# Kernel tuning notes

Hardware: AMD Instinct MI355X
Metric: run time of the kernel (lower is better)

## Reference

```python
import jax, jax.numpy as jnp
import numpy as np

EPS = 0.0  # GIN epsilon (train_eps=False)

def setup_inputs() -> dict:
    key = jax.random.key(0)
    k_x, k_e, k_w1, k_w2 = jax.random.split(key, 4)
    N, E, D = 100000, 625000, 128
    x = jax.random.normal(k_x, (N, D), dtype=jnp.float32)
    edge_index = jax.random.randint(k_e, (2, E), 0, N, dtype=jnp.int32)
    s = 1.0 / np.sqrt(D)
    W1 = jax.random.normal(k_w1, (D, D), dtype=jnp.float32) * s
    b1 = jnp.zeros((D,), dtype=jnp.float32)
    W2 = jax.random.normal(k_w2, (D, D), dtype=jnp.float32) * s
    b2 = jnp.zeros((D,), dtype=jnp.float32)
    return {"x": x, "edge_index": edge_index, "W1": W1, "b1": b1, "W2": W2, "b2": b2}

def reference(x, edge_index, W1, b1, W2, b2):
    # GINConv: out_i = MLP((1+eps)*x_i + sum_{j in N(i)} x_j)
    src = edge_index[0]
    dst = edge_index[1]
    agg = jax.ops.segment_sum(x[src], dst, num_segments=x.shape[0])  # [N, D]
    h = (1.0 + EPS) * x + agg
    # MLP: Linear -> ReLU -> Dropout(eval: identity) -> Linear
    h = jax.nn.relu(h @ W1.T + b1)
    h = h @ W2.T + b2
    # outer activation; outer dropout is identity in eval
    return jax.nn.relu(h)
```

## Files before the change

kernel.cpp:

```cpp
#include <hip/hip_runtime.h>


#define D 128
#define HLD 136
#define CPIT 40
#define KSLOT 32
#define CSTR 32

typedef __attribute__((ext_vector_type(8))) short bf16x8;
typedef __attribute__((ext_vector_type(4))) float f32x4;

__device__ __forceinline__ short f2bf(float f) {
    union { float f; unsigned u; } v; v.f = f;
    unsigned r = v.u + 0x7fffu + ((v.u >> 16) & 1u);
    return (short)(r >> 16);
}
__device__ __forceinline__ float bflo(unsigned u) {
    union { unsigned u; float f; } v; v.u = u << 16; return v.f;
}
__device__ __forceinline__ float bfhi(unsigned u) {
    union { unsigned u; float f; } v; v.u = u & 0xffff0000u; return v.f;
}
__device__ __forceinline__ unsigned pack2(float a, float b) {
    return ((unsigned)(unsigned short)f2bf(a)) | (((unsigned)(unsigned short)f2bf(b)) << 16);
}

__global__ __launch_bounds__(256) void convert_fill(const float4* __restrict__ x4,
                                                    unsigned short* __restrict__ xb,
                                                    const int* __restrict__ ei,
                                                    int* __restrict__ cnt,
                                                    int* __restrict__ bucket,
                                                    int nConv, int nFillBlocks, int E) {
    if ((int)blockIdx.x < nFillBlocks) {
        int t8 = blockIdx.x * 256 + threadIdx.x;
        int E8 = E >> 3;
        if (t8 < E8) {
            const int4* ei4 = (const int4*)ei;
            int E4 = E >> 2;
            int4 s0 = ei4[2 * t8],      s1 = ei4[2 * t8 + 1];
            int4 d0 = ei4[E4 + 2 * t8], d1 = ei4[E4 + 2 * t8 + 1];
            int sl;
            sl = atomicAdd(&cnt[d0.x * CSTR], 1); if (sl < KSLOT) bucket[d0.x * KSLOT + sl] = s0.x;
            sl = atomicAdd(&cnt[d0.y * CSTR], 1); if (sl < KSLOT) bucket[d0.y * KSLOT + sl] = s0.y;
            sl = atomicAdd(&cnt[d0.z * CSTR], 1); if (sl < KSLOT) bucket[d0.z * KSLOT + sl] = s0.z;
            sl = atomicAdd(&cnt[d0.w * CSTR], 1); if (sl < KSLOT) bucket[d0.w * KSLOT + sl] = s0.w;
            sl = atomicAdd(&cnt[d1.x * CSTR], 1); if (sl < KSLOT) bucket[d1.x * KSLOT + sl] = s1.x;
            sl = atomicAdd(&cnt[d1.y * CSTR], 1); if (sl < KSLOT) bucket[d1.y * KSLOT + sl] = s1.y;
            sl = atomicAdd(&cnt[d1.z * CSTR], 1); if (sl < KSLOT) bucket[d1.z * KSLOT + sl] = s1.z;
            sl = atomicAdd(&cnt[d1.w * CSTR], 1); if (sl < KSLOT) bucket[d1.w * KSLOT + sl] = s1.w;
        }
    } else {
        int t = ((int)blockIdx.x - nFillBlocks) * 256 + threadIdx.x;
        if (t < nConv) {
            float4 a = x4[2 * t], b = x4[2 * t + 1];
            bf16x8 r;
            r[0] = f2bf(a.x); r[1] = f2bf(a.y); r[2] = f2bf(a.z); r[3] = f2bf(a.w);
            r[4] = f2bf(b.x); r[5] = f2bf(b.y); r[6] = f2bf(b.z); r[7] = f2bf(b.w);
            ((bf16x8*)xb)[t] = r;
        }
    }
}

__global__ __launch_bounds__(256) void gather_kernel(const uint4* __restrict__ xb4,
                                                     const int* __restrict__ cnt,
                                                     const int* __restrict__ bucket,
                                                     uint4* __restrict__ h04, int N) {
    int g = blockIdx.x * 256 + threadIdx.x;
    int node = g >> 4;
    if (node >= N) return;
    int lane = g & 15;
    int deg = cnt[node * CSTR];
    deg = deg < KSLOT ? deg : KSLOT;
    const int bb = node * KSLOT;

    uint4 sv = xb4[node * 16 + lane];
    float a0 = bflo(sv.x), a1 = bfhi(sv.x), a2 = bflo(sv.y), a3 = bfhi(sv.y);
    float a4 = bflo(sv.z), a5 = bfhi(sv.z), a6 = bflo(sv.w), a7 = bfhi(sv.w);

    int e = 0;
    for (; e + 3 < deg; e += 4) {
        int s0 = bucket[bb + e], s1 = bucket[bb + e + 1];
        int s2 = bucket[bb + e + 2], s3 = bucket[bb + e + 3];
        uint4 p0 = xb4[s0 * 16 + lane];
        uint4 p1 = xb4[s1 * 16 + lane];
        uint4 p2 = xb4[s2 * 16 + lane];
        uint4 p3 = xb4[s3 * 16 + lane];
        a0 += bflo(p0.x) + bflo(p1.x) + bflo(p2.x) + bflo(p3.x);
        a1 += bfhi(p0.x) + bfhi(p1.x) + bfhi(p2.x) + bfhi(p3.x);
        a2 += bflo(p0.y) + bflo(p1.y) + bflo(p2.y) + bflo(p3.y);
        a3 += bfhi(p0.y) + bfhi(p1.y) + bfhi(p2.y) + bfhi(p3.y);
        a4 += bflo(p0.z) + bflo(p1.z) + bflo(p2.z) + bflo(p3.z);
        a5 += bfhi(p0.z) + bfhi(p1.z) + bfhi(p2.z) + bfhi(p3.z);
        a6 += bflo(p0.w) + bflo(p1.w) + bflo(p2.w) + bflo(p3.w);
        a7 += bfhi(p0.w) + bfhi(p1.w) + bfhi(p2.w) + bfhi(p3.w);
    }
    for (; e < deg; ++e) {
        uint4 p = xb4[bucket[bb + e] * 16 + lane];
        a0 += bflo(p.x); a1 += bfhi(p.x); a2 += bflo(p.y); a3 += bfhi(p.y);
        a4 += bflo(p.z); a5 += bfhi(p.z); a6 += bflo(p.w); a7 += bfhi(p.w);
    }
    uint4 r;
    r.x = pack2(a0, a1);
    r.y = pack2(a2, a3);
    r.z = pack2(a4, a5);
    r.w = pack2(a6, a7);
    h04[node * 16 + lane] = r;
}

__global__ __launch_bounds__(512, 4) void mlp_fused(const short* __restrict__ h0,
                                                    const float* __restrict__ W1,
                                                    const float* __restrict__ b1,
                                                    const float* __restrict__ W2,
                                                    const float* __restrict__ b2,
                                                    float* __restrict__ out, int N) {
    __shared__ short W1l[D * HLD];
    __shared__ short W2l[D * HLD];
    __shared__ short chunk[8 * 16 * CPIT];

    {
        const float4* W14 = (const float4*)W1;
        const float4* W24 = (const float4*)W2;
        for (int idx = threadIdx.x; idx < D * (D / 4); idx += 512) {
            int n = idx >> 5;
            int k4 = idx & 31;
            float4 w = W14[idx];
            short* dp = &W1l[n * HLD + k4 * 4];
            dp[0] = f2bf(w.x); dp[1] = f2bf(w.y); dp[2] = f2bf(w.z); dp[3] = f2bf(w.w);
            w = W24[idx];
            dp = &W2l[n * HLD + k4 * 4];
            dp[0] = f2bf(w.x); dp[1] = f2bf(w.y); dp[2] = f2bf(w.z); dp[3] = f2bf(w.w);
        }
    }
    __syncthreads();

    const int wave = threadIdx.x >> 6;
    const int lane = threadIdx.x & 63;
    const int m = lane & 15;
    const int quad = lane >> 4;
    const int tiles = (N + 127) / 128;
    short* ch = &chunk[wave * 16 * CPIT];

    float b1r[8], b2r[8];
#pragma unroll
    for (int j = 0; j < 8; ++j) { b1r[j] = b1[j * 16 + m]; b2r[j] = b2[j * 16 + m]; }

    for (int t = blockIdx.x; t < tiles; t += gridDim.x) {
        const int r0 = t * 128 + wave * 16;
        const int arow = r0 + m;

        bf16x8 afrag[4];
        if (arow < N) {
#pragma unroll
            for (int ks = 0; ks < 4; ++ks)
                afrag[ks] = *(const bf16x8*)&h0[(long long)arow * D + ks * 32 + quad * 8];
        } else {
#pragma unroll
            for (int ks = 0; ks < 4; ++ks) afrag[ks] = (bf16x8)(short)0;
        }

        f32x4 acc2[8];
#pragma unroll
        for (int jt = 0; jt < 8; ++jt) acc2[jt] = (f32x4)0.0f;

#pragma unroll
        for (int ks2 = 0; ks2 < 4; ++ks2) {
            f32x4 acc1[2];
            acc1[0] = (f32x4)0.0f;
            acc1[1] = (f32x4)0.0f;
#pragma unroll
            for (int half = 0; half < 2; ++half) {
                int jt = 2 * ks2 + half;
#pragma unroll
                for (int ks = 0; ks < 4; ++ks) {
                    bf16x8 b = *(const bf16x8*)&W1l[(jt * 16 + m) * HLD + ks * 32 + quad * 8];
                    acc1[half] = __builtin_amdgcn_mfma_f32_16x16x32_bf16(afrag[ks], b, acc1[half], 0, 0, 0);
                }
            }
#pragma unroll
            for (int half = 0; half < 2; ++half) {
                float bv = b1r[2 * ks2 + half];
#pragma unroll
                for (int i = 0; i < 4; ++i) {
                    float v = acc1[half][i] + bv;
                    v = v > 0.0f ? v : 0.0f;
                    ch[(quad * 4 + i) * CPIT + half * 16 + m] = f2bf(v);
                }
            }
            bf16x8 a2 = *(const bf16x8*)&ch[m * CPIT + quad * 8];
#pragma unroll
            for (int jt2 = 0; jt2 < 8; ++jt2) {
                bf16x8 b = *(const bf16x8*)&W2l[(jt2 * 16 + m) * HLD + ks2 * 32 + quad * 8];
                acc2[jt2] = __builtin_amdgcn_mfma_f32_16x16x32_bf16(a2, b, acc2[jt2], 0, 0, 0);
            }
        }

#pragma unroll
        for (int jt2 = 0; jt2 < 8; ++jt2) {
            int col = jt2 * 16 + m;
            float bv = b2r[jt2];
#pragma unroll
            for (int i = 0; i < 4; ++i) {
                int row = r0 + quad * 4 + i;
                if (row < N) {
                    float v = acc2[jt2][i] + bv;
                    v = v > 0.0f ? v : 0.0f;
                    __builtin_nontemporal_store(v, &out[(long long)row * D + col]);
                }
            }
        }
    }
}

extern "C" void kernel_launch(void* const* d_in, const int* in_sizes, int n_in,
                              void* d_out, int out_size, void* d_ws, size_t ws_size,
                              hipStream_t stream) {
    const float* x  = (const float*)d_in[0];
    const int*   ei = (const int*)d_in[1];
    const float* W1 = (const float*)d_in[2];
    const float* b1 = (const float*)d_in[3];
    const float* W2 = (const float*)d_in[4];
    const float* b2 = (const float*)d_in[5];
    float* out = (float*)d_out;

    const int N = in_sizes[0] / D;
    const int E = in_sizes[1] / 2;

    unsigned short* h0 = (unsigned short*)d_ws;
    unsigned short* xb = h0 + (size_t)N * D;
    int* cnt    = (int*)(xb + (size_t)N * D);
    int* bucket = cnt + (size_t)N * CSTR;

    hipMemsetAsync(cnt, 0, (size_t)N * CSTR * sizeof(int), stream);

    {
        int nConv = N * (D / 8);
        int nConvBlocks = (nConv + 255) / 256;
        int nFillBlocks = ((E >> 3) + 255) / 256;
        convert_fill<<<nFillBlocks + nConvBlocks, 256, 0, stream>>>(
            (const float4*)x, xb, ei, cnt, bucket, nConv, nFillBlocks, E);
    }

    {
        long long thr = (long long)N * 16;
        gather_kernel<<<(int)((thr + 255) / 256), 256, 0, stream>>>(
            (const uint4*)xb, cnt, bucket, (uint4*)h0, N);
    }

    mlp_fused<<<512, 512, 0, stream>>>((const short*)h0, W1, b1, W2, b2, out, N);
}
```

Baseline: 193.1 us.

## Fuse neighbor gather-aggregation into MLP kernel, dropping intermediate h0 buffer

Removes the separate gather kernel and performs the neighbor sum directly inside the MLP kernel, building each lane's A-fragment from bucketed neighbor rows before the MFMA stages. This drops the write and re-read of the bf16 h0 intermediate and one kernel launch. In exchange the gather now runs at the MLP kernel's occupancy (512 blocks of 512 threads with large LDS), so fewer loads are in flight to hide the latency of random memory accesses. It also adds 32 float accumulators per lane, which raises register pressure.

```diff
diff --git a/kernel.cpp b/kernel.cpp
--- a/kernel.cpp
+++ b/kernel.cpp
@@ -20,9 +20,6 @@
 }
 __device__ __forceinline__ float bfhi(unsigned u) {
     union { unsigned u; float f; } v; v.u = u & 0xffff0000u; return v.f;
-}
-__device__ __forceinline__ unsigned pack2(float a, float b) {
-    return ((unsigned)(unsigned short)f2bf(a)) | (((unsigned)(unsigned short)f2bf(b)) << 16);
 }
 
 __global__ __launch_bounds__(256) void convert_fill(const float4* __restrict__ x4,
@@ -61,58 +58,14 @@
     }
 }
 
-__global__ __launch_bounds__(256) void gather_kernel(const uint4* __restrict__ xb4,
+__global__ __launch_bounds__(512, 4) void gather_mlp(const uint4* __restrict__ xb4,
                                                      const int* __restrict__ cnt,
                                                      const int* __restrict__ bucket,
-                                                     uint4* __restrict__ h04, int N) {
-    int g = blockIdx.x * 256 + threadIdx.x;
-    int node = g >> 4;
-    if (node >= N) return;
-    int lane = g & 15;
-    int deg = cnt[node * CSTR];
-    deg = deg < KSLOT ? deg : KSLOT;
-    const int bb = node * KSLOT;
-
-    uint4 sv = xb4[node * 16 + lane];
-    float a0 = bflo(sv.x), a1 = bfhi(sv.x), a2 = bflo(sv.y), a3 = bfhi(sv.y);
-    float a4 = bflo(sv.z), a5 = bfhi(sv.z), a6 = bflo(sv.w), a7 = bfhi(sv.w);
-
-    int e = 0;
-    for (; e + 3 < deg; e += 4) {
-        int s0 = bucket[bb + e], s1 = bucket[bb + e + 1];
-        int s2 = bucket[bb + e + 2], s3 = bucket[bb + e + 3];
-        uint4 p0 = xb4[s0 * 16 + lane];
-        uint4 p1 = xb4[s1 * 16 + lane];
-        uint4 p2 = xb4[s2 * 16 + lane];
-        uint4 p3 = xb4[s3 * 16 + lane];
-        a0 += bflo(p0.x) + bflo(p1.x) + bflo(p2.x) + bflo(p3.x);
-        a1 += bfhi(p0.x) + bfhi(p1.x) + bfhi(p2.x) + bfhi(p3.x);
-        a2 += bflo(p0.y) + bflo(p1.y) + bflo(p2.y) + bflo(p3.y);
-        a3 += bfhi(p0.y) + bfhi(p1.y) + bfhi(p2.y) + bfhi(p3.y);
-        a4 += bflo(p0.z) + bflo(p1.z) + bflo(p2.z) + bflo(p3.z);
-        a5 += bfhi(p0.z) + bfhi(p1.z) + bfhi(p2.z) + bfhi(p3.z);
-        a6 += bflo(p0.w) + bflo(p1.w) + bflo(p2.w) + bflo(p3.w);
-        a7 += bfhi(p0.w) + bfhi(p1.w) + bfhi(p2.w) + bfhi(p3.w);
-    }
-    for (; e < deg; ++e) {
-        uint4 p = xb4[bucket[bb + e] * 16 + lane];
-        a0 += bflo(p.x); a1 += bfhi(p.x); a2 += bflo(p.y); a3 += bfhi(p.y);
-        a4 += bflo(p.z); a5 += bfhi(p.z); a6 += bflo(p.w); a7 += bfhi(p.w);
-    }
-    uint4 r;
-    r.x = pack2(a0, a1);
-    r.y = pack2(a2, a3);
-    r.z = pack2(a4, a5);
-    r.w = pack2(a6, a7);
-    h04[node * 16 + lane] = r;
-}
-
-__global__ __launch_bounds__(512, 4) void mlp_fused(const short* __restrict__ h0,
-                                                    const float* __restrict__ W1,
-                                                    const float* __restrict__ b1,
-                                                    const float* __restrict__ W2,
-                                                    const float* __restrict__ b2,
-                                                    float* __restrict__ out, int N) {
+                                                     const float* __restrict__ W1,
+                                                     const float* __restrict__ b1,
+                                                     const float* __restrict__ W2,
+                                                     const float* __restrict__ b2,
+                                                     float* __restrict__ out, int N) {
     __shared__ short W1l[D * HLD];
     __shared__ short W2l[D * HLD];
     __shared__ short chunk[8 * 16 * CPIT];
@@ -146,13 +99,60 @@
 
     for (int t = blockIdx.x; t < tiles; t += gridDim.x) {
         const int r0 = t * 128 + wave * 16;
-        const int arow = r0 + m;
+        const int node = r0 + m;
 
         bf16x8 afrag[4];
-        if (arow < N) {
-#pragma unroll
-            for (int ks = 0; ks < 4; ++ks)
-                afrag[ks] = *(const bf16x8*)&h0[(long long)arow * D + ks * 32 + quad * 8];
+        if (node < N) {
+            float a[32];
+            const uint4* xrow = xb4 + (size_t)node * 16;
+#pragma unroll
+            for (int ks = 0; ks < 4; ++ks) {
+                uint4 p = xrow[4 * ks + quad];
+                a[ks * 8 + 0] = bflo(p.x); a[ks * 8 + 1] = bfhi(p.x);
+                a[ks * 8 + 2] = bflo(p.y); a[ks * 8 + 3] = bfhi(p.y);
+                a[ks * 8 + 4] = bflo(p.z); a[ks * 8 + 5] = bfhi(p.z);
+                a[ks * 8 + 6] = bflo(p.w); a[ks * 8 + 7] = bfhi(p.w);
+            }
+            int deg = cnt[node * CSTR];
+            deg = deg < KSLOT ? deg : KSLOT;
+            const int bb = node * KSLOT;
+            int e = 0;
+            for (; e + 1 < deg; e += 2) {
+                int s0 = bucket[bb + e], s1 = bucket[bb + e + 1];
+                const uint4* q0 = xb4 + (size_t)s0 * 16;
+                const uint4* q1 = xb4 + (size_t)s1 * 16;
+#pragma unroll
+                for (int ks = 0; ks < 4; ++ks) {
+                    uint4 p0 = q0[4 * ks + quad];
+                    uint4 p1 = q1[4 * ks + quad];
+                    a[ks * 8 + 0] += bflo(p0.x) + bflo(p1.x);
+                    a[ks * 8 + 1] += bfhi(p0.x) + bfhi(p1.x);
+                    a[ks * 8 + 2] += bflo(p0.y) + bflo(p1.y);
+                    a[ks * 8 + 3] += bfhi(p0.y) + bfhi(p1.y);
+                    a[ks * 8 + 4] += bflo(p0.z) + bflo(p1.z);
+                    a[ks * 8 + 5] += bfhi(p0.z) + bfhi(p1.z);
+                    a[ks * 8 + 6] += bflo(p0.w) + bflo(p1.w);
+                    a[ks * 8 + 7] += bfhi(p0.w) + bfhi(p1.w);
+                }
+            }
+            if (e < deg) {
+                const uint4* q0 = xb4 + (size_t)bucket[bb + e] * 16;
+#pragma unroll
+                for (int ks = 0; ks < 4; ++ks) {
+                    uint4 p0 = q0[4 * ks + quad];
+                    a[ks * 8 + 0] += bflo(p0.x); a[ks * 8 + 1] += bfhi(p0.x);
+                    a[ks * 8 + 2] += bflo(p0.y); a[ks * 8 + 3] += bfhi(p0.y);
+                    a[ks * 8 + 4] += bflo(p0.z); a[ks * 8 + 5] += bfhi(p0.z);
+                    a[ks * 8 + 6] += bflo(p0.w); a[ks * 8 + 7] += bfhi(p0.w);
+                }
+            }
+#pragma unroll
+            for (int ks = 0; ks < 4; ++ks) {
+                bf16x8 r;
+#pragma unroll
+                for (int j = 0; j < 8; ++j) r[j] = f2bf(a[ks * 8 + j]);
+                afrag[ks] = r;
+            }
         } else {
 #pragma unroll
             for (int ks = 0; ks < 4; ++ks) afrag[ks] = (bf16x8)(short)0;
@@ -225,8 +225,7 @@
     const int N = in_sizes[0] / D;
     const int E = in_sizes[1] / 2;
 
-    unsigned short* h0 = (unsigned short*)d_ws;
-    unsigned short* xb = h0 + (size_t)N * D;
+    unsigned short* xb = (unsigned short*)d_ws;
     int* cnt    = (int*)(xb + (size_t)N * D);
     int* bucket = cnt + (size_t)N * CSTR;
 
@@ -240,11 +239,6 @@
             (const float4*)x, xb, ei, cnt, bucket, nConv, nFillBlocks, E);
     }
 
-    {
-        long long thr = (long long)N * 16;
-        gather_kernel<<<(int)((thr + 255) / 256), 256, 0, stream>>>(
-            (const uint4*)xb, cnt, bucket, (uint4*)h0, N);
-    }
-
-    mlp_fused<<<512, 512, 0, stream>>>((const short*)h0, W1, b1, W2, b2, out, N);
-}
+    gather_mlp<<<512, 512, 0, stream>>>((const uint4*)xb, cnt, bucket,
+                                        W1, b1, W2, b2, out, N);
+}
```

After: 200.9 us (median of 2 runs). 1.04x slower.
